# Kernel optimization log

Hardware: AMD Instinct MI355X
Metric: run time of the kernel (lower is better)

The kernel has to match this reference:

```python
import jax, jax.numpy as jnp
import numpy as np

B = 4            # number of scenes (equal-size segments; offset = [M,2M,3M,4M])
K_NEAR = 16
K_FAR = 32
K_SMOOTH = 8
T_LOC = 0.1
T_CON = 0.5
BN_EPS = 1e-5


def setup_inputs() -> dict:
    key = jax.random.key(0)
    ks = jax.random.split(key, 8)
    N, C, H, O = 32768, 6, 64, 1
    coords = jax.random.uniform(ks[0], (N, 3), jnp.float32) * 2.0 - 1.0
    feat = jax.random.normal(ks[1], (N, C), jnp.float32)
    return {
        'feat': feat,
        'coords': coords,
        'W1': jax.random.normal(ks[2], (C, H), jnp.float32) * 0.1,
        'b1': jnp.zeros((H,), jnp.float32),
        'g1': jnp.ones((H,), jnp.float32),
        'be1': jnp.zeros((H,), jnp.float32),
        'W2': jax.random.normal(ks[3], (H, H), jnp.float32) * 0.1,
        'b2': jnp.zeros((H,), jnp.float32),
        'g2': jnp.ones((H,), jnp.float32),
        'be2': jnp.zeros((H,), jnp.float32),
        'W3': jax.random.normal(ks[4], (H, O), jnp.float32) * 0.1,
        'b3': jnp.zeros((O,), jnp.float32),
    }


def _bn_train(x, g, b):
    # BatchNorm1d in train mode: biased batch statistics
    mu = x.mean(axis=0)
    var = x.var(axis=0)
    return g * (x - mu) * jax.lax.rsqrt(var + BN_EPS) + b


def _knn_per_scene(c):
    # c: [M,3] -> [M,K_FAR] sorted nearest-neighbor indices (self first)
    sq = jnp.sum(c * c, axis=-1)                       # [M]
    d2 = sq[:, None] + sq[None, :] - 2.0 * (c @ c.T)   # [M,M] GEMM-based
    return jax.lax.top_k(-d2, K_FAR)[1]                # [M,K_FAR]


def _forward(feat, coords, W1, b1, g1, be1, W2, b2, g2, be2, W3, b3):
    N = feat.shape[0]
    M = N // B
    # ---- PointSorter MLP -> ordering scores in (0,1) ----
    h = jax.nn.gelu(_bn_train(feat @ W1 + b1, g1, be1), approximate=False)
    h = jax.nn.gelu(_bn_train(h @ W2 + b2, g2, be2), approximate=False)
    scores = jax.nn.sigmoid(h @ W3 + b3)               # [N, num_orders]
    s = scores.mean(axis=1, keepdims=True)             # [N,1] (scores_mean)
    # ---- single fused KNN (k=32); slice for k=16 (near) and k=8 (smooth) ----
    cb = coords.reshape(B, M, 3)
    idx = jax.vmap(_knn_per_scene)(cb)                 # [B,M,K_FAR] local
    idx = (idx + (jnp.arange(B) * M)[:, None, None]).reshape(N, K_FAR)
    idx_near = idx[:, :K_NEAR]
    idx_far = idx[:, K_NEAR:]
    idx_sm = idx[:, :K_SMOOTH]
    # ---- locality: neighbors should have similar scores ----
    sd = jnp.abs(s[:, None, :] - s[idx_near])[..., 0]          # [N,16]
    diff = coords[:, None, :] - coords[idx_near]               # [N,16,3]
    d = jnp.sqrt(jnp.maximum(jnp.sum(diff * diff, axis=2), 1e-24))
    w = jnp.exp(-d / T_LOC)
    loss_loc = jnp.sum(w * sd * sd) / jnp.maximum(jnp.sum(w), 1e-8)
    # ---- contrastive: far points should have different scores ----
    sim_pos = 1.0 - jnp.abs(s[:, None, :] - s[idx_near])       # [N,16,1]
    sim_neg = 1.0 - jnp.abs(s[:, None, :] - s[idx_far])        # [N,16,1]
    loss_pos = -jnp.mean(jnp.log(jax.nn.sigmoid(sim_pos / T_CON) + 1e-8))
    loss_neg = -jnp.mean(jnp.log(1.0 - jax.nn.sigmoid(sim_neg / T_CON) + 1e-8))
    loss_con = loss_pos + loss_neg
    # ---- smoothness: score close to mean of 8-NN scores ----
    nmean = s[idx_sm].mean(axis=1)                             # [N,1]
    loss_sm = jnp.mean((s - nmean) ** 2)
    return 1.0 * loss_loc + 0.5 * loss_con + 0.2 * loss_sm


def reference(feat, coords, W1, b1, g1, be1, W2, b2, g2, be2, W3, b3):
    return _forward(feat, coords, W1, b1, g1, be1, W2, b2, g2, be2, W3, b3)
```

## Files before the change

### kernel.cpp

```cpp
#include <hip/hip_runtime.h>

typedef unsigned long long u64;
typedef unsigned int u32;
typedef unsigned short u16;

#define N_PTS 32768
#define M_PTS 8192
#define C_IN 6
#define H_DIM 64

#define G 6
#define NCELL 216
#define NCELL_T 864
#define CW (1.0f/3.0f)

#define QPP 32
#define TPQ 8
#define CH 512
#define CAP 112
#define CAPP 113

#define TL0 0.0494f
#define TL1 0.0740f
#define TL2 0.1110f
#define TL3 0.1736f
#define TL4 0.2600f
#define TL5 0.4000f


__device__ __forceinline__ float gelu_exact(float x) {
    return 0.5f * x * (1.0f + erff(x * 0.70710678118654752f));
}
__device__ __forceinline__ float sigmoidf_(float x) {
    return 1.0f / (1.0f + expf(-x));
}

__global__ __launch_bounds__(256) void k_cellpack(const float* __restrict__ coords,
        u32* __restrict__ gcount, u16* __restrict__ pcell) {
    int n = blockIdx.x * 256 + threadIdx.x;
    float x = coords[n*3], y = coords[n*3+1], z = coords[n*3+2];
    int cx = min(G-1, max(0, (int)floorf((x + 1.0f) * 3.0f)));
    int cy = min(G-1, max(0, (int)floorf((y + 1.0f) * 3.0f)));
    int cz = min(G-1, max(0, (int)floorf((z + 1.0f) * 3.0f)));
    int scene = n >> 13;
    int gcid = scene * NCELL + (cz*G + cy)*G + cx;
    pcell[n] = (u16)gcid;
    atomicAdd(&gcount[gcid], 1u);
}

__global__ __launch_bounds__(256) void k_scan(const u32* __restrict__ gcount,
        u32* __restrict__ cellstart, u32* __restrict__ cellptr) {
    __shared__ u32 sc[256];
    int t = threadIdx.x;
    u32 loc[4]; u32 s = 0;
    #pragma unroll
    for (int j = 0; j < 4; ++j) {
        int idx = t*4 + j;
        loc[j] = (idx < NCELL_T) ? gcount[idx] : 0u;
        s += loc[j];
    }
    sc[t] = s;
    __syncthreads();
    for (int off = 1; off < 256; off <<= 1) {
        u32 v = sc[t];
        if (t >= off) v += sc[t-off];
        __syncthreads();
        sc[t] = v;
        __syncthreads();
    }
    u32 run = sc[t] - s;
    #pragma unroll
    for (int j = 0; j < 4; ++j) {
        int idx = t*4 + j;
        if (idx < NCELL_T) { cellstart[idx] = run; cellptr[idx] = run; }
        run += loc[j];
    }
    if (t == 255) cellstart[NCELL_T] = sc[255];
}

__global__ __launch_bounds__(256) void k_scatter(const float* __restrict__ coords,
        const u16* __restrict__ pcell, u32* __restrict__ cellptr,
        float4* __restrict__ P4s, u16* __restrict__ meta) {
    int n = blockIdx.x * 256 + threadIdx.x;
    float x = coords[n*3], y = coords[n*3+1], z = coords[n*3+2];
    float sq = fmaf(x, x, fmaf(y, y, z*z));
    u32 pos = atomicAdd(&cellptr[pcell[n]], 1u);
    P4s[pos] = make_float4(x, y, z, sq);
    meta[pos] = (u16)(n & (M_PTS-1));
}

__global__ __launch_bounds__(256) void k_l1stats(const float* __restrict__ feat,
        const float* __restrict__ W1, const float* __restrict__ b1,
        float* __restrict__ stats) {
    __shared__ float sW[C_IN*H_DIM];
    __shared__ float red[2][4][H_DIM];
    int t = threadIdx.x;
    for (int i = t; i < C_IN*H_DIM; i += 256) sW[i] = W1[i];
    __syncthreads();
    int c = t & 63, r = t >> 6;
    float bias = b1[c];
    float s1 = 0.f, s2 = 0.f;
    for (int n = blockIdx.x*4 + r; n < N_PTS; n += 1024) {
        const float* f = feat + n*C_IN;
        float h = bias;
        #pragma unroll
        for (int k = 0; k < C_IN; ++k) h = fmaf(f[k], sW[k*H_DIM + c], h);
        s1 += h; s2 = fmaf(h, h, s2);
    }
    red[0][r][c] = s1; red[1][r][c] = s2;
    __syncthreads();
    if (t < 64) {
        float a = red[0][0][t]+red[0][1][t]+red[0][2][t]+red[0][3][t];
        float b = red[1][0][t]+red[1][1][t]+red[1][2][t]+red[1][3][t];
        atomicAdd(&stats[t], a);
        atomicAdd(&stats[64+t], b);
    }
}

__global__ __launch_bounds__(256) void k_l2(const float* __restrict__ feat,
        const float* __restrict__ W1, const float* __restrict__ b1,
        const float* __restrict__ stats1, const float* __restrict__ g1,
        const float* __restrict__ be1, const float* __restrict__ W2,
        const float* __restrict__ b2, float* __restrict__ stats) {
    __shared__ float sW1[C_IN*H_DIM];
    __shared__ float sW2[H_DIM*H_DIM];
    __shared__ float sA[4][H_DIM];
    __shared__ float red[2][4][H_DIM];
    int t = threadIdx.x;
    for (int i = t; i < C_IN*H_DIM; i += 256) sW1[i] = W1[i];
    for (int i = t; i < H_DIM*H_DIM; i += 256) sW2[i] = W2[i];
    __syncthreads();
    int c = t & 63, r = t >> 6;
    float mean1 = stats1[c] * (1.0f/N_PTS);
    float var1  = stats1[64+c] * (1.0f/N_PTS) - mean1*mean1;
    float sc1 = g1[c] * rsqrtf(var1 + 1e-5f);
    float sh1 = be1[c] - mean1*sc1;
    float bias1 = b1[c], bias2 = b2[c];
    float s1 = 0.f, s2 = 0.f;
    for (int n0 = blockIdx.x*4; n0 < N_PTS; n0 += 1024) {
        int n = n0 + r;
        const float* f = feat + n*C_IN;
        float h = bias1;
        #pragma unroll
        for (int k = 0; k < C_IN; ++k) h = fmaf(f[k], sW1[k*H_DIM+c], h);
        float a = gelu_exact(fmaf(sc1, h, sh1));
        __syncthreads();
        sA[r][c] = a;
        __syncthreads();
        float h2 = bias2;
        #pragma unroll
        for (int k = 0; k < H_DIM; ++k) h2 = fmaf(sA[r][k], sW2[k*H_DIM+c], h2);
        s1 += h2; s2 = fmaf(h2, h2, s2);
    }
    red[0][r][c] = s1; red[1][r][c] = s2;
    __syncthreads();
    if (t < 64) {
        float a = red[0][0][t]+red[0][1][t]+red[0][2][t]+red[0][3][t];
        float b = red[1][0][t]+red[1][1][t]+red[1][2][t]+red[1][3][t];
        atomicAdd(&stats[t], a);
        atomicAdd(&stats[64+t], b);
    }
}

__global__ __launch_bounds__(256) void k_score(const float* __restrict__ feat,
        const float* __restrict__ W1, const float* __restrict__ b1,
        const float* __restrict__ stats1, const float* __restrict__ g1,
        const float* __restrict__ be1, const float* __restrict__ W2,
        const float* __restrict__ b2, const float* __restrict__ stats2,
        const float* __restrict__ g2v, const float* __restrict__ be2,
        const float* __restrict__ W3, const float* __restrict__ b3,
        float* __restrict__ S) {
    __shared__ float sW1[C_IN*H_DIM];
    __shared__ float sW2[H_DIM*H_DIM];
    __shared__ float sA[4][H_DIM];
    int t = threadIdx.x;
    for (int i = t; i < C_IN*H_DIM; i += 256) sW1[i] = W1[i];
    for (int i = t; i < H_DIM*H_DIM; i += 256) sW2[i] = W2[i];
    __syncthreads();
    int c = t & 63, r = t >> 6;
    float mean1 = stats1[c] * (1.0f/N_PTS);
    float var1  = stats1[64+c] * (1.0f/N_PTS) - mean1*mean1;
    float sc1 = g1[c] * rsqrtf(var1 + 1e-5f);
    float sh1 = be1[c] - mean1*sc1;
    float mean2 = stats2[c] * (1.0f/N_PTS);
    float var2  = stats2[64+c] * (1.0f/N_PTS) - mean2*mean2;
    float sc2 = g2v[c] * rsqrtf(var2 + 1e-5f);
    float sh2 = be2[c] - mean2*sc2;
    float bias1 = b1[c], bias2 = b2[c], w3 = W3[c], bb = b3[0];
    for (int n0 = blockIdx.x*4; n0 < N_PTS; n0 += 1024) {
        int n = n0 + r;
        const float* f = feat + n*C_IN;
        float h = bias1;
        #pragma unroll
        for (int k = 0; k < C_IN; ++k) h = fmaf(f[k], sW1[k*H_DIM+c], h);
        float a = gelu_exact(fmaf(sc1, h, sh1));
        __syncthreads();
        sA[r][c] = a;
        __syncthreads();
        float h2 = bias2;
        #pragma unroll
        for (int k = 0; k < H_DIM; ++k) h2 = fmaf(sA[r][k], sW2[k*H_DIM+c], h2);
        float a2 = gelu_exact(fmaf(sc2, h2, sh2));
        float v = a2 * w3;
        #pragma unroll
        for (int m = 32; m; m >>= 1) v += __shfl_xor(v, m, 64);
        if (c == 0) S[n] = sigmoidf_(v + bb);
    }
}

__global__ __launch_bounds__(256) void k_knn(const float4* __restrict__ P4s,
        const u16* __restrict__ meta, const u32* __restrict__ cellstart,
        const float* __restrict__ S, double* __restrict__ blockloss) {
    __shared__ float4 tile[CH];
    __shared__ u16 tmeta[CH];
    __shared__ u64 buf[QPP][CAPP];
    __shared__ u32 cnts[QPP][6];
    __shared__ float tauA[QPP];
    __shared__ u32 ccount[QPP];
    __shared__ int runb[16], rune[16], nruns_s;
    __shared__ double lred[4][5];

    int t = threadIdx.x;
    int bid = blockIdx.x;
    int scene = bid / NCELL;
    int cid = bid - scene*NCELL;
    int cx = cid % G, cy = (cid / G) % G, cz = cid / (G*G);
    int sbase = scene * M_PTS;

    int cc[3] = {cx, cy, cz};
    bool wall[3]; int W = 0;
    #pragma unroll
    for (int d = 0; d < 3; ++d) { wall[d] = (cc[d] == 0 || cc[d] == G-1); W += wall[d]; }
    int lo[3], hi[3];
    #pragma unroll
    for (int d = 0; d < 3; ++d) {
        if (W >= 2 && !wall[d]) { lo[d] = min(max(cc[d]-2, 0), G-5); hi[d] = lo[d]+4; }
        else                    { lo[d] = min(max(cc[d]-1, 0), G-3); hi[d] = lo[d]+2; }
    }
    float lof[3], hif[3]; bool lw[3], hw[3];
    #pragma unroll
    for (int d = 0; d < 3; ++d) {
        lof[d] = -1.0f + lo[d]*CW; hif[d] = -1.0f + (hi[d]+1)*CW;
        lw[d] = (lo[d] == 0); hw[d] = (hi[d] == G-1);
    }

    if (t == 0) {
        int nr = 0;
        int nx = hi[0]-lo[0]+1;
        for (int z = lo[2]; z <= hi[2]; ++z)
            for (int y = lo[1]; y <= hi[1]; ++y) {
                int bc = scene*NCELL + (z*G + y)*G + lo[0];
                runb[nr] = (int)cellstart[bc];
                rune[nr] = (int)cellstart[bc + nx];
                ++nr;
            }
        nruns_s = nr;
    }
    int gcid = scene*NCELL + cid;
    int qstart = (int)cellstart[gcid];
    int qn = (int)cellstart[gcid+1] - qstart;
    __syncthreads();
    int nruns = nruns_s;

    double anum=0.0, aden=0.0, aslp=0.0, asln=0.0, asm_=0.0;

    for (int p0 = 0; p0 < qn; p0 += QPP) {
        int qpp = min(QPP, qn - p0);
        int q = t & (QPP-1);
        int lane8 = t >> 5;
        bool qact = q < qpp;
        int qi = qact ? q : (qpp-1);
        float4 qc = P4s[qstart + p0 + qi];
        float qsq = qc.w;
        float qd[3] = {qc.x, qc.y, qc.z};
        float cov = 1e9f;
        #pragma unroll
        for (int d = 0; d < 3; ++d) {
            if (!lw[d]) cov = fminf(cov, qd[d] - lof[d]);
            if (!hw[d]) cov = fminf(cov, hif[d] - qd[d]);
        }
        float g2 = cov*cov;
        float tp0 = TL0-qsq, tp1 = TL1-qsq, tp2 = TL2-qsq,
              tp3 = TL3-qsq, tp4 = TL4-qsq, tp5 = TL5-qsq;
        u32 c0=0,c1=0,c2=0,c3=0,c4=0,c5=0;

        for (int r = 0; r < nruns; ++r) {
            for (int off = runb[r]; off < rune[r]; off += CH) {
                int cnum = min(CH, rune[r] - off);
                __syncthreads();
                for (int j = t; j < cnum; j += 256) {
                    tile[j] = P4s[off + j];
                    tmeta[j] = meta[off + j];
                }
                __syncthreads();
                for (int i = lane8; i < cnum; i += TPQ) {
                    float4 p = tile[i];
                    float dot = fmaf(qc.x, p.x, fmaf(qc.y, p.y, qc.z*p.z));
                    float e2 = fmaf(-2.0f, dot, p.w);
                    c0 += (e2 < tp0); c1 += (e2 < tp1); c2 += (e2 < tp2);
                    c3 += (e2 < tp3); c4 += (e2 < tp4); c5 += (e2 < tp5);
                }
            }
        }
        __syncthreads();
        if (t < QPP*6) ((u32*)cnts)[t] = 0;
        if (t < QPP) ccount[t] = 0;
        __syncthreads();
        if (qact) {
            atomicAdd(&cnts[q][0], c0); atomicAdd(&cnts[q][1], c1);
            atomicAdd(&cnts[q][2], c2); atomicAdd(&cnts[q][3], c3);
            atomicAdd(&cnts[q][4], c4); atomicAdd(&cnts[q][5], c5);
        }
        __syncthreads();
        if (t < QPP) {
            float tau = TL2;
            if (TL3 <= g2) tau = TL3;
            if (TL4 <= g2) tau = TL4;
            if (TL5 <= g2) tau = TL5;
            if      (cnts[t][0] >= 32) tau = TL0;
            else if (cnts[t][1] >= 32) tau = TL1;
            else if (cnts[t][2] >= 32) tau = TL2;
            else if (TL3 <= g2 && cnts[t][3] >= 32) tau = TL3;
            else if (TL4 <= g2 && cnts[t][4] >= 32) tau = TL4;
            else if (TL5 <= g2 && cnts[t][5] >= 32) tau = TL5;
            tauA[t] = tau;
        }
        __syncthreads();
        float taup = tauA[q] - qsq;

        for (int r = 0; r < nruns; ++r) {
            for (int off = runb[r]; off < rune[r]; off += CH) {
                int cnum = min(CH, rune[r] - off);
                __syncthreads();
                for (int j = t; j < cnum; j += 256) {
                    tile[j] = P4s[off + j];
                    tmeta[j] = meta[off + j];
                }
                __syncthreads();
                int lbase = off - sbase;
                for (int i = lane8; i < cnum; i += TPQ) {
                    float4 p = tile[i];
                    float dot = fmaf(qc.x, p.x, fmaf(qc.y, p.y, qc.z*p.z));
                    float e2 = fmaf(-2.0f, dot, p.w);
                    if (qact && e2 < taup) {
                        float d2 = fmaxf(e2 + qsq, 0.0f);
                        u32 lm = (u32)tmeta[i];
                        u64 key = ((u64)__float_as_uint(d2) << 32)
                                | (lm << 13) | (u32)(lbase + i);
                        u32 pos = atomicAdd(&ccount[q], 1u);
                        if (pos < CAP) buf[q][pos] = key;
                    }
                }
            }
        }
        __syncthreads();

        int tq = t >> 3, l8 = t & 7;
        bool ract = tq < qpp;
        int qs = qstart + p0 + (ract ? tq : 0);
        float4 qf = P4s[qs];
        int qg = sbase + (int)meta[qs];
        float si = S[qg];
        u32 Mq = ract ? min(ccount[tq], (u32)CAP) : 0u;
        double num=0.0, den=0.0, slp=0.0, sln=0.0;
        float smsum = 0.f;
        for (u32 i = l8; i < Mq; i += 8) {
            u64 key = buf[tq][i];
            u32 rank = 0;
            for (u32 j = 0; j < Mq; ++j) rank += (buf[tq][j] < key);
            if (rank < 32) {
                u32 jl = (u32)(key & 0x1FFFu);
                u32 jo = (u32)((key >> 13) & 0x1FFFu);
                float sj = S[sbase + (int)jo];
                float4 cj = P4s[sbase + (int)jl];
                float sd = fabsf(si - sj);
                float sim = 1.0f - sd;
                if (rank < 16) {
                    float dx = qf.x-cj.x, dy = qf.y-cj.y, dz = qf.z-cj.z;
                    float d2 = fmaf(dx,dx,fmaf(dy,dy,dz*dz));
                    float d = sqrtf(fmaxf(d2, 1e-24f));
                    float w = expf(-10.0f*d);
                    num += (double)(w*sd*sd);
                    den += (double)w;
                    slp += (double)logf(sigmoidf_(2.0f*sim) + 1e-8f);
                    if (rank < 8) smsum += sj;
                } else {
                    sln += (double)logf(sigmoidf_(-2.0f*sim) + 1e-8f);
                }
            }
        }
        #pragma unroll
        for (int m = 4; m; m >>= 1) smsum += __shfl_xor(smsum, m, 64);
        anum += num; aden += den; aslp += slp; asln += sln;
        if (l8 == 0 && ract) {
            float dd = si - smsum*0.125f;
            asm_ += (double)(dd*dd);
        }
        __syncthreads();
    }

    double v[5] = {anum, aden, aslp, asln, asm_};
    #pragma unroll
    for (int k = 0; k < 5; ++k) {
        for (int m = 32; m; m >>= 1) v[k] += __shfl_xor(v[k], m, 64);
    }
    int wave = t >> 6;
    if ((t & 63) == 0) {
        #pragma unroll
        for (int k = 0; k < 5; ++k) lred[wave][k] = v[k];
    }
    __syncthreads();
    if (t == 0) {
        #pragma unroll
        for (int k = 0; k < 5; ++k)
            blockloss[(size_t)bid*5 + k] =
                lred[0][k] + lred[1][k] + lred[2][k] + lred[3][k];
    }
}

__global__ __launch_bounds__(256) void k_final(const double* __restrict__ blockloss,
                                               float* __restrict__ out) {
    __shared__ double red[256][5];
    int t = threadIdx.x;
    double v[5] = {0,0,0,0,0};
    for (int i = t; i < NCELL_T; i += 256) {
        #pragma unroll
        for (int k = 0; k < 5; ++k) v[k] += blockloss[(size_t)i*5 + k];
    }
    #pragma unroll
    for (int k = 0; k < 5; ++k) red[t][k] = v[k];
    __syncthreads();
    for (int s = 128; s; s >>= 1) {
        if (t < s) {
            #pragma unroll
            for (int k = 0; k < 5; ++k) red[t][k] += red[t+s][k];
        }
        __syncthreads();
    }
    if (t == 0) {
        double num = red[0][0], den = red[0][1], slp = red[0][2],
               sln = red[0][3], ssm = red[0][4];
        double loss_loc = num / fmax(den, 1e-8);
        double inv = 1.0 / ((double)N_PTS * 16.0);
        double loss_con = -(slp * inv) - (sln * inv);
        double loss_sm = ssm / (double)N_PTS;
        out[0] = (float)(loss_loc + 0.5*loss_con + 0.2*loss_sm);
    }
}

extern "C" void kernel_launch(void* const* d_in, const int* in_sizes, int n_in,
                              void* d_out, int out_size, void* d_ws, size_t ws_size,
                              hipStream_t stream) {
    const float* feat   = (const float*)d_in[0];
    const float* coords = (const float*)d_in[1];
    const float* W1 = (const float*)d_in[2];
    const float* b1 = (const float*)d_in[3];
    const float* g1 = (const float*)d_in[4];
    const float* be1= (const float*)d_in[5];
    const float* W2 = (const float*)d_in[6];
    const float* b2 = (const float*)d_in[7];
    const float* g2 = (const float*)d_in[8];
    const float* be2= (const float*)d_in[9];
    const float* W3 = (const float*)d_in[10];
    const float* b3 = (const float*)d_in[11];

    char* ws = (char*)d_ws;
    float* stats1   = (float*)(ws);
    float* stats2   = (float*)(ws + 512);
    u32* gcount     = (u32*)(ws + 1024);
    u32* cellstart  = (u32*)(ws + 4480);
    u32* cellptr    = (u32*)(ws + 7944);
    double* blockloss = (double*)(ws + 11408);
    float* S        = (float*)(ws + 45968);
    float4* P4s     = (float4*)(ws + 177040);
    u16* pcell      = (u16*)(ws + 701328);
    u16* meta       = (u16*)(ws + 766864);

    hipMemsetAsync(d_ws, 0, 4480, stream);

    hipLaunchKernelGGL(k_cellpack, dim3(128), dim3(256), 0, stream, coords, gcount, pcell);
    hipLaunchKernelGGL(k_scan,     dim3(1),   dim3(256), 0, stream, gcount, cellstart, cellptr);
    hipLaunchKernelGGL(k_scatter,  dim3(128), dim3(256), 0, stream, coords, pcell, cellptr, P4s, meta);
    hipLaunchKernelGGL(k_l1stats,  dim3(256), dim3(256), 0, stream, feat, W1, b1, stats1);
    hipLaunchKernelGGL(k_l2,       dim3(256), dim3(256), 0, stream,
                       feat, W1, b1, stats1, g1, be1, W2, b2, stats2);
    hipLaunchKernelGGL(k_score,    dim3(256), dim3(256), 0, stream,
                       feat, W1, b1, stats1, g1, be1, W2, b2, stats2, g2, be2, W3, b3, S);
    hipLaunchKernelGGL(k_knn,      dim3(NCELL_T), dim3(256), 0, stream,
                       P4s, meta, cellstart, S, blockloss);
    hipLaunchKernelGGL(k_final,    dim3(1),   dim3(256), 0, stream, blockloss, (float*)d_out);
}
```

Before: 360.5 us.

## Drop LDS staging in KNN scan, use register weights and shuffles in MLP

The MLP kernels now keep weight columns in registers and broadcast activations with wave shuffles, which removes the shared-memory weight copies and the per-iteration block barriers. The KNN kernel drops its LDS tile staging and reads candidate points straight from global memory (cache-served), with one query per lane (64 queries per block) and four waves striding over the candidates. The rank-selection phase now has each thread rank eight keys at once against the buffer, cutting repeated LDS reads. The candidate buffer capacity shrinks from 112 to 96, which saves LDS but raises the risk of overflow truncation, and the per-thread register pressure goes up (64-float weight arrays).

```diff
diff --git a/kernel.cpp b/kernel.cpp
--- a/kernel.cpp
+++ b/kernel.cpp
@@ -14,11 +14,9 @@
 #define NCELL_T 864
 #define CW (1.0f/3.0f)
 
-#define QPP 32
-#define TPQ 8
-#define CH 512
-#define CAP 112
-#define CAPP 113
+#define QPP 64
+#define CAP 96
+#define CAPP 97
 
 #define TL0 0.0494f
 #define TL1 0.0740f
@@ -92,19 +90,20 @@
 __global__ __launch_bounds__(256) void k_l1stats(const float* __restrict__ feat,
         const float* __restrict__ W1, const float* __restrict__ b1,
         float* __restrict__ stats) {
-    __shared__ float sW[C_IN*H_DIM];
     __shared__ float red[2][4][H_DIM];
     int t = threadIdx.x;
-    for (int i = t; i < C_IN*H_DIM; i += 256) sW[i] = W1[i];
-    __syncthreads();
     int c = t & 63, r = t >> 6;
+    float w1c[C_IN];
+    #pragma unroll
+    for (int k = 0; k < C_IN; ++k) w1c[k] = W1[k*H_DIM + c];
     float bias = b1[c];
     float s1 = 0.f, s2 = 0.f;
+    #pragma unroll 1
     for (int n = blockIdx.x*4 + r; n < N_PTS; n += 1024) {
         const float* f = feat + n*C_IN;
         float h = bias;
         #pragma unroll
-        for (int k = 0; k < C_IN; ++k) h = fmaf(f[k], sW[k*H_DIM + c], h);
+        for (int k = 0; k < C_IN; ++k) h = fmaf(f[k], w1c[k], h);
         s1 += h; s2 = fmaf(h, h, s2);
     }
     red[0][r][c] = s1; red[1][r][c] = s2;
@@ -122,37 +121,35 @@
         const float* __restrict__ stats1, const float* __restrict__ g1,
         const float* __restrict__ be1, const float* __restrict__ W2,
         const float* __restrict__ b2, float* __restrict__ stats) {
-    __shared__ float sW1[C_IN*H_DIM];
-    __shared__ float sW2[H_DIM*H_DIM];
-    __shared__ float sA[4][H_DIM];
     __shared__ float red[2][4][H_DIM];
     int t = threadIdx.x;
-    for (int i = t; i < C_IN*H_DIM; i += 256) sW1[i] = W1[i];
-    for (int i = t; i < H_DIM*H_DIM; i += 256) sW2[i] = W2[i];
-    __syncthreads();
-    int c = t & 63, r = t >> 6;
+    int c = t & 63, w = t >> 6;
+    float w2c[H_DIM];
+    #pragma unroll
+    for (int k = 0; k < H_DIM; ++k) w2c[k] = W2[k*H_DIM + c];
+    float w1c[C_IN];
+    #pragma unroll
+    for (int k = 0; k < C_IN; ++k) w1c[k] = W1[k*H_DIM + c];
     float mean1 = stats1[c] * (1.0f/N_PTS);
     float var1  = stats1[64+c] * (1.0f/N_PTS) - mean1*mean1;
     float sc1 = g1[c] * rsqrtf(var1 + 1e-5f);
     float sh1 = be1[c] - mean1*sc1;
     float bias1 = b1[c], bias2 = b2[c];
     float s1 = 0.f, s2 = 0.f;
-    for (int n0 = blockIdx.x*4; n0 < N_PTS; n0 += 1024) {
-        int n = n0 + r;
+    int gw = blockIdx.x*4 + w;
+    #pragma unroll 1
+    for (int n = gw; n < N_PTS; n += 1024) {
         const float* f = feat + n*C_IN;
         float h = bias1;
         #pragma unroll
-        for (int k = 0; k < C_IN; ++k) h = fmaf(f[k], sW1[k*H_DIM+c], h);
+        for (int k = 0; k < C_IN; ++k) h = fmaf(f[k], w1c[k], h);
         float a = gelu_exact(fmaf(sc1, h, sh1));
-        __syncthreads();
-        sA[r][c] = a;
-        __syncthreads();
         float h2 = bias2;
         #pragma unroll
-        for (int k = 0; k < H_DIM; ++k) h2 = fmaf(sA[r][k], sW2[k*H_DIM+c], h2);
+        for (int k = 0; k < H_DIM; ++k) h2 = fmaf(__shfl(a, k, 64), w2c[k], h2);
         s1 += h2; s2 = fmaf(h2, h2, s2);
     }
-    red[0][r][c] = s1; red[1][r][c] = s2;
+    red[0][w][c] = s1; red[1][w][c] = s2;
     __syncthreads();
     if (t < 64) {
         float a = red[0][0][t]+red[0][1][t]+red[0][2][t]+red[0][3][t];
@@ -170,14 +167,14 @@
         const float* __restrict__ g2v, const float* __restrict__ be2,
         const float* __restrict__ W3, const float* __restrict__ b3,
         float* __restrict__ S) {
-    __shared__ float sW1[C_IN*H_DIM];
-    __shared__ float sW2[H_DIM*H_DIM];
-    __shared__ float sA[4][H_DIM];
-    int t = threadIdx.x;
-    for (int i = t; i < C_IN*H_DIM; i += 256) sW1[i] = W1[i];
-    for (int i = t; i < H_DIM*H_DIM; i += 256) sW2[i] = W2[i];
-    __syncthreads();
-    int c = t & 63, r = t >> 6;
+    int t = threadIdx.x;
+    int c = t & 63, w = t >> 6;
+    float w2c[H_DIM];
+    #pragma unroll
+    for (int k = 0; k < H_DIM; ++k) w2c[k] = W2[k*H_DIM + c];
+    float w1c[C_IN];
+    #pragma unroll
+    for (int k = 0; k < C_IN; ++k) w1c[k] = W1[k*H_DIM + c];
     float mean1 = stats1[c] * (1.0f/N_PTS);
     float var1  = stats1[64+c] * (1.0f/N_PTS) - mean1*mean1;
     float sc1 = g1[c] * rsqrtf(var1 + 1e-5f);
@@ -187,19 +184,17 @@
     float sc2 = g2v[c] * rsqrtf(var2 + 1e-5f);
     float sh2 = be2[c] - mean2*sc2;
     float bias1 = b1[c], bias2 = b2[c], w3 = W3[c], bb = b3[0];
-    for (int n0 = blockIdx.x*4; n0 < N_PTS; n0 += 1024) {
-        int n = n0 + r;
+    int gw = blockIdx.x*4 + w;
+    #pragma unroll 1
+    for (int n = gw; n < N_PTS; n += 1024) {
         const float* f = feat + n*C_IN;
         float h = bias1;
         #pragma unroll
-        for (int k = 0; k < C_IN; ++k) h = fmaf(f[k], sW1[k*H_DIM+c], h);
+        for (int k = 0; k < C_IN; ++k) h = fmaf(f[k], w1c[k], h);
         float a = gelu_exact(fmaf(sc1, h, sh1));
-        __syncthreads();
-        sA[r][c] = a;
-        __syncthreads();
         float h2 = bias2;
         #pragma unroll
-        for (int k = 0; k < H_DIM; ++k) h2 = fmaf(sA[r][k], sW2[k*H_DIM+c], h2);
+        for (int k = 0; k < H_DIM; ++k) h2 = fmaf(__shfl(a, k, 64), w2c[k], h2);
         float a2 = gelu_exact(fmaf(sc2, h2, sh2));
         float v = a2 * w3;
         #pragma unroll
@@ -207,17 +202,22 @@
         if (c == 0) S[n] = sigmoidf_(v + bb);
     }
 }
+
+#define CNT6(pp) { \
+    float dot = fmaf(qc.x, (pp).x, fmaf(qc.y, (pp).y, qc.z*(pp).z)); \
+    float e2 = fmaf(-2.0f, dot, (pp).w); \
+    c0 += (e2 < tp0); c1 += (e2 < tp1); c2 += (e2 < tp2); \
+    c3 += (e2 < tp3); c4 += (e2 < tp4); c5 += (e2 < tp5); }
 
 __global__ __launch_bounds__(256) void k_knn(const float4* __restrict__ P4s,
         const u16* __restrict__ meta, const u32* __restrict__ cellstart,
         const float* __restrict__ S, double* __restrict__ blockloss) {
-    __shared__ float4 tile[CH];
-    __shared__ u16 tmeta[CH];
     __shared__ u64 buf[QPP][CAPP];
     __shared__ u32 cnts[QPP][6];
     __shared__ float tauA[QPP];
     __shared__ u32 ccount[QPP];
-    __shared__ int runb[16], rune[16], nruns_s;
+    __shared__ int runb[16], rune[16];
+    __shared__ int nruns_s;
     __shared__ double lred[4][5];
 
     int t = threadIdx.x;
@@ -227,15 +227,15 @@
     int cx = cid % G, cy = (cid / G) % G, cz = cid / (G*G);
     int sbase = scene * M_PTS;
 
-    int cc[3] = {cx, cy, cz};
+    int ccrd[3] = {cx, cy, cz};
     bool wall[3]; int W = 0;
     #pragma unroll
-    for (int d = 0; d < 3; ++d) { wall[d] = (cc[d] == 0 || cc[d] == G-1); W += wall[d]; }
+    for (int d = 0; d < 3; ++d) { wall[d] = (ccrd[d] == 0 || ccrd[d] == G-1); W += wall[d]; }
     int lo[3], hi[3];
     #pragma unroll
     for (int d = 0; d < 3; ++d) {
-        if (W >= 2 && !wall[d]) { lo[d] = min(max(cc[d]-2, 0), G-5); hi[d] = lo[d]+4; }
-        else                    { lo[d] = min(max(cc[d]-1, 0), G-3); hi[d] = lo[d]+2; }
+        if (W >= 2 && !wall[d]) { lo[d] = min(max(ccrd[d]-2, 0), G-5); hi[d] = lo[d]+4; }
+        else                    { lo[d] = min(max(ccrd[d]-1, 0), G-3); hi[d] = lo[d]+2; }
     }
     float lof[3], hif[3]; bool lw[3], hw[3];
     #pragma unroll
@@ -262,18 +262,16 @@
     __syncthreads();
     int nruns = nruns_s;
 
+    int q = t & 63, w4 = t >> 6;
     double anum=0.0, aden=0.0, aslp=0.0, asln=0.0, asm_=0.0;
 
     for (int p0 = 0; p0 < qn; p0 += QPP) {
         int qpp = min(QPP, qn - p0);
-        int q = t & (QPP-1);
-        int lane8 = t >> 5;
         bool qact = q < qpp;
-        int qi = qact ? q : (qpp-1);
-        float4 qc = P4s[qstart + p0 + qi];
+        float4 qc = P4s[qstart + p0 + (qact ? q : qpp-1)];
         float qsq = qc.w;
+        float cov = 1e9f;
         float qd[3] = {qc.x, qc.y, qc.z};
-        float cov = 1e9f;
         #pragma unroll
         for (int d = 0; d < 3; ++d) {
             if (!lw[d]) cov = fminf(cov, qd[d] - lof[d]);
@@ -285,22 +283,13 @@
         u32 c0=0,c1=0,c2=0,c3=0,c4=0,c5=0;
 
         for (int r = 0; r < nruns; ++r) {
-            for (int off = runb[r]; off < rune[r]; off += CH) {
-                int cnum = min(CH, rune[r] - off);
-                __syncthreads();
-                for (int j = t; j < cnum; j += 256) {
-                    tile[j] = P4s[off + j];
-                    tmeta[j] = meta[off + j];
-                }
-                __syncthreads();
-                for (int i = lane8; i < cnum; i += TPQ) {
-                    float4 p = tile[i];
-                    float dot = fmaf(qc.x, p.x, fmaf(qc.y, p.y, qc.z*p.z));
-                    float e2 = fmaf(-2.0f, dot, p.w);
-                    c0 += (e2 < tp0); c1 += (e2 < tp1); c2 += (e2 < tp2);
-                    c3 += (e2 < tp3); c4 += (e2 < tp4); c5 += (e2 < tp5);
-                }
-            }
+            int pe = rune[r];
+            int p = runb[r] + w4;
+            for (; p + 12 < pe; p += 16) {
+                float4 a0 = P4s[p], a1 = P4s[p+4], a2 = P4s[p+8], a3 = P4s[p+12];
+                CNT6(a0); CNT6(a1); CNT6(a2); CNT6(a3);
+            }
+            for (; p < pe; p += 4) { float4 a0 = P4s[p]; CNT6(a0); }
         }
         __syncthreads();
         if (t < QPP*6) ((u32*)cnts)[t] = 0;
@@ -329,70 +318,74 @@
         float taup = tauA[q] - qsq;
 
         for (int r = 0; r < nruns; ++r) {
-            for (int off = runb[r]; off < rune[r]; off += CH) {
-                int cnum = min(CH, rune[r] - off);
-                __syncthreads();
-                for (int j = t; j < cnum; j += 256) {
-                    tile[j] = P4s[off + j];
-                    tmeta[j] = meta[off + j];
+            int pe = rune[r];
+            for (int p = runb[r] + w4; p < pe; p += 4) {
+                float4 pp = P4s[p];
+                float dot = fmaf(qc.x, pp.x, fmaf(qc.y, pp.y, qc.z*pp.z));
+                float e2 = fmaf(-2.0f, dot, pp.w);
+                if (qact && e2 < taup) {
+                    float d2 = fmaxf(e2 + qsq, 0.0f);
+                    u32 lm = (u32)meta[p];
+                    u64 key = ((u64)__float_as_uint(d2) << 32)
+                            | ((u64)lm << 13) | (u32)(p - sbase);
+                    u32 pos = atomicAdd(&ccount[q], 1u);
+                    if (pos < CAP) buf[q][pos] = key;
                 }
-                __syncthreads();
-                int lbase = off - sbase;
-                for (int i = lane8; i < cnum; i += TPQ) {
-                    float4 p = tile[i];
-                    float dot = fmaf(qc.x, p.x, fmaf(qc.y, p.y, qc.z*p.z));
-                    float e2 = fmaf(-2.0f, dot, p.w);
-                    if (qact && e2 < taup) {
-                        float d2 = fmaxf(e2 + qsq, 0.0f);
-                        u32 lm = (u32)tmeta[i];
-                        u64 key = ((u64)__float_as_uint(d2) << 32)
-                                | (lm << 13) | (u32)(lbase + i);
-                        u32 pos = atomicAdd(&ccount[q], 1u);
-                        if (pos < CAP) buf[q][pos] = key;
+            }
+        }
+        __syncthreads();
+
+        int tq = t >> 2, l4 = t & 3;
+        bool ract = tq < qpp;
+        u32 Mq = ract ? min(ccount[tq], (u32)CAP) : 0u;
+        int qs = qstart + p0 + (ract ? tq : 0);
+        float4 qf = P4s[qs];
+        float si = S[sbase + (int)meta[qs]];
+        double num=0.0, den=0.0, slp=0.0, sln=0.0;
+        float smsum = 0.f;
+        u32 perT = (Mq > (u32)l4) ? ((Mq - (u32)l4 + 3u) >> 2) : 0u;
+        for (u32 cb = 0; cb < perT; cb += 8) {
+            u32 cnt = min(8u, perT - cb);
+            u64 myk[8]; u32 rk[8];
+            #pragma unroll
+            for (int k = 0; k < 8; ++k) {
+                myk[k] = (k < (int)cnt) ? buf[tq][l4 + 4*(cb + (u32)k)] : ~0ull;
+                rk[k] = 0;
+            }
+            for (u32 j = 0; j < Mq; ++j) {
+                u64 kj = buf[tq][j];
+                #pragma unroll
+                for (int k = 0; k < 8; ++k) rk[k] += (kj < myk[k]);
+            }
+            #pragma unroll
+            for (int k = 0; k < 8; ++k) {
+                if (k < (int)cnt && rk[k] < 32) {
+                    u64 key = myk[k];
+                    u32 jl = (u32)(key & 0x1FFFu);
+                    u32 jo = (u32)((key >> 13) & 0x1FFFu);
+                    float sj = S[sbase + (int)jo];
+                    float sd = fabsf(si - sj);
+                    float sim = 1.0f - sd;
+                    if (rk[k] < 16) {
+                        float4 cj = P4s[sbase + (int)jl];
+                        float dx = qf.x-cj.x, dy = qf.y-cj.y, dz = qf.z-cj.z;
+                        float d2 = fmaf(dx,dx,fmaf(dy,dy,dz*dz));
+                        float d = sqrtf(fmaxf(d2, 1e-24f));
+                        float wgt = expf(-10.0f*d);
+                        num += (double)(wgt*sd*sd);
+                        den += (double)wgt;
+                        slp += (double)logf(sigmoidf_(2.0f*sim) + 1e-8f);
+                        if (rk[k] < 8) smsum += sj;
+                    } else {
+                        sln += (double)logf(sigmoidf_(-2.0f*sim) + 1e-8f);
                     }
                 }
             }
         }
-        __syncthreads();
-
-        int tq = t >> 3, l8 = t & 7;
-        bool ract = tq < qpp;
-        int qs = qstart + p0 + (ract ? tq : 0);
-        float4 qf = P4s[qs];
-        int qg = sbase + (int)meta[qs];
-        float si = S[qg];
-        u32 Mq = ract ? min(ccount[tq], (u32)CAP) : 0u;
-        double num=0.0, den=0.0, slp=0.0, sln=0.0;
-        float smsum = 0.f;
-        for (u32 i = l8; i < Mq; i += 8) {
-            u64 key = buf[tq][i];
-            u32 rank = 0;
-            for (u32 j = 0; j < Mq; ++j) rank += (buf[tq][j] < key);
-            if (rank < 32) {
-                u32 jl = (u32)(key & 0x1FFFu);
-                u32 jo = (u32)((key >> 13) & 0x1FFFu);
-                float sj = S[sbase + (int)jo];
-                float4 cj = P4s[sbase + (int)jl];
-                float sd = fabsf(si - sj);
-                float sim = 1.0f - sd;
-                if (rank < 16) {
-                    float dx = qf.x-cj.x, dy = qf.y-cj.y, dz = qf.z-cj.z;
-                    float d2 = fmaf(dx,dx,fmaf(dy,dy,dz*dz));
-                    float d = sqrtf(fmaxf(d2, 1e-24f));
-                    float w = expf(-10.0f*d);
-                    num += (double)(w*sd*sd);
-                    den += (double)w;
-                    slp += (double)logf(sigmoidf_(2.0f*sim) + 1e-8f);
-                    if (rank < 8) smsum += sj;
-                } else {
-                    sln += (double)logf(sigmoidf_(-2.0f*sim) + 1e-8f);
-                }
-            }
-        }
-        #pragma unroll
-        for (int m = 4; m; m >>= 1) smsum += __shfl_xor(smsum, m, 64);
+        smsum += __shfl_xor(smsum, 1, 64);
+        smsum += __shfl_xor(smsum, 2, 64);
         anum += num; aden += den; aslp += slp; asln += sln;
-        if (l8 == 0 && ract) {
+        if (ract && l4 == 0) {
             float dd = si - smsum*0.125f;
             asm_ += (double)(dd*dd);
         }
```

Result: slower. 395.7 us (+9.8%).
